# Kernel tuning notes

Measured on AMD Instinct MI355X. Metric: run time of the kernel, lower is better.

The kernel has to match this reference:

```python
import jax, jax.numpy as jnp
import numpy as np

B, C, L = 4, 256, 4096
C8 = C // 8

def setup_inputs() -> dict:
    key = jax.random.key(0)
    ks = jax.random.split(key, 8)
    s = 1.0 / np.sqrt(C)
    x = jax.random.normal(ks[0], (B, C, L), dtype=jnp.float32)
    Wq = jax.random.normal(ks[1], (C8, C), dtype=jnp.float32) * s
    bq = jax.random.normal(ks[2], (C8,), dtype=jnp.float32) * s
    Wk = jax.random.normal(ks[3], (C8, C), dtype=jnp.float32) * s
    bk = jax.random.normal(ks[4], (C8,), dtype=jnp.float32) * s
    Wv = jax.random.normal(ks[5], (C, C), dtype=jnp.float32) * s
    bv = jax.random.normal(ks[6], (C,), dtype=jnp.float32) * s
    gamma = jax.random.normal(ks[7], (1,), dtype=jnp.float32) * 0.1
    return {"x": x, "Wq": Wq, "bq": bq, "Wk": Wk, "bk": bk, "Wv": Wv, "bv": bv, "gamma": gamma}

def reference(x, Wq, bq, Wk, bk, Wv, bv, gamma):
    # pointwise conv1d == channel matmul: [O,C] x [B,C,L] -> [B,O,L]
    q = jnp.einsum('oc,bcl->bol', Wq, x) + bq[None, :, None]   # [B, C8, L]
    k = jnp.einsum('oc,bcl->bol', Wk, x) + bk[None, :, None]   # [B, C8, L]
    v = jnp.einsum('oc,bcl->bol', Wv, x) + bv[None, :, None]   # [B, C,  L]
    # attention[b,i,j] = sum_c q[b,c,i] * k[b,c,j]
    attn = jnp.einsum('bci,bcj->bij', q, k)                    # [B, L, L]
    attn = jax.nn.softmax(attn, axis=-1)
    # out[b,c,i] = sum_j v[b,c,j] * attn[b,i,j]
    out = jnp.einsum('bcj,bij->bci', v, attn)                  # [B, C, L]
    return gamma * out + x
```

## Files before the change

kernel.cpp:

```cpp
#include <hip/hip_runtime.h>
#include <math.h>

#define BB 4
#define CC 256
#define LL 4096
#define DD 32
#define LOG2E 1.44269504088896f

typedef __attribute__((ext_vector_type(8))) short short8;
typedef __attribute__((ext_vector_type(4))) short short4v;
typedef __attribute__((ext_vector_type(4))) float f32x4;
typedef __attribute__((ext_vector_type(4))) unsigned int uint4v;
typedef __attribute__((ext_vector_type(2))) unsigned int uint2v;

#define BARRIER() asm volatile("s_waitcnt lgkmcnt(0)\n\ts_barrier" ::: "memory")

__device__ inline unsigned short f2bf(float f) {
  union { float f; unsigned u; } v; v.f = f;
  unsigned r = v.u + 0x7fffu + ((v.u >> 16) & 1u);
  return (unsigned short)(r >> 16);
}

__device__ inline float fast_exp2(float x) {
#if __has_builtin(__builtin_amdgcn_exp2f)
  return __builtin_amdgcn_exp2f(x);
#else
  return exp2f(x);
#endif
}

__device__ __host__ inline int sigma32(int p) {
  const int q4 = (p >> 3) & 3, u = p & 7;
  return 16 * (u >> 2) + 4 * q4 + (u & 3);
}

__global__ __launch_bounds__(256) void wprep_kernel(
    const float* __restrict__ Wq, const float* __restrict__ Wk, const float* __restrict__ Wv,
    unsigned short* __restrict__ wf)
{
  const int t = threadIdx.x;
  const int ot = blockIdx.x >> 1;
  const int rep = blockIdx.x & 1;
  const int lane = t & 63, cl = lane & 15, q4 = lane >> 4;
  const int ks = (t >> 6) + 4 * rep;
  const int o = ot * 16 + cl;
  const int c = ks * 32 + q4 * 8;
  const float* src = (o < 32) ? (Wq + o * CC) : (o < 64) ? (Wk + (o - 32) * CC)
                                              : (Wv + (o - 64) * CC);
  const float sc = (o < 32) ? LOG2E : 1.0f;
  unsigned short p[8];
  #pragma unroll
  for (int j = 0; j < 8; ++j) p[j] = f2bf(src[c + j] * sc);
  uint4v u;
  u.x = (unsigned)p[0] | ((unsigned)p[1] << 16);
  u.y = (unsigned)p[2] | ((unsigned)p[3] << 16);
  u.z = (unsigned)p[4] | ((unsigned)p[5] << 16);
  u.w = (unsigned)p[6] | ((unsigned)p[7] << 16);
  *(uint4v*)(wf + ((size_t)(ot * 8 + ks) * 64 + lane) * 8) = u;
}

__global__ __launch_bounds__(512, 4) void qkv_kernel(
    const float* __restrict__ x, const unsigned short* __restrict__ wf,
    const float* __restrict__ bq, const float* __restrict__ bk, const float* __restrict__ bv,
    unsigned short* __restrict__ qT, unsigned short* __restrict__ kT,
    unsigned short* __restrict__ vf)
{
  __shared__ union {
    float xl[32 * 261];
    struct {
      unsigned short qk[32 * 72];
      __align__(16) unsigned short v[256 * 40];
    } ep;
  } sm;

  const int t = threadIdx.x;
  const int lane = t & 63, cl = lane & 15, q4 = lane >> 4;
  const int blk = blockIdx.x;
  const int b  = (blk & 7) >> 1;
  const int it = ((blk >> 3) << 1) + (blk & 1);
  const int i0 = it * 32;

  {
    const int ln8 = t & 7;
    #pragma unroll
    for (int p = 0; p < 4; ++p) {
      const int c = (t >> 3) + 64 * p;
      const f32x4 v = *(const f32x4*)(x + ((size_t)(b * CC + c)) * LL + i0 + ln8 * 4);
      #pragma unroll
      for (int k = 0; k < 4; ++k) sm.xl[(ln8 * 4 + k) * 261 + c] = v[k];
    }
  }
  __syncthreads();

  const int wi = (t >> 6) & 1, wo = t >> 7;
  const f32x4 zero = {0.f, 0.f, 0.f, 0.f};
  f32x4 acc[5];
  #pragma unroll
  for (int u = 0; u < 5; ++u) acc[u] = zero;

  for (int ks = 0; ks < 8; ++ks) {
    unsigned short p[8];
    #pragma unroll
    for (int j = 0; j < 8; ++j)
      p[j] = f2bf(sm.xl[(16 * wi + cl) * 261 + ks * 32 + q4 * 8 + j]);
    union { short8 s; uint4v u; } bfr;
    bfr.u.x = (unsigned)p[0] | ((unsigned)p[1] << 16);
    bfr.u.y = (unsigned)p[2] | ((unsigned)p[3] << 16);
    bfr.u.z = (unsigned)p[4] | ((unsigned)p[5] << 16);
    bfr.u.w = (unsigned)p[6] | ((unsigned)p[7] << 16);
    #pragma unroll
    for (int u = 0; u < 5; ++u) {
      const short8 a = *(const short8*)(wf + ((size_t)((wo * 5 + u) * 8 + ks) * 64 + lane) * 8);
      acc[u] = __builtin_amdgcn_mfma_f32_16x16x32_bf16(a, bfr.s, acc[u], 0, 0, 0);
    }
  }
  __syncthreads();

  #pragma unroll
  for (int u = 0; u < 5; ++u) {
    const int g = wo * 5 + u;
    if (g < 4) {
      short4v pk;
      #pragma unroll
      for (int r = 0; r < 4; ++r) {
        const int o = 16 * g + 4 * q4 + r;
        const float v = acc[u][r] + ((o < 32) ? bq[o] * LOG2E : bk[o - 32]);
        pk[r] = (short)f2bf(v);
      }
      *(short4v*)&sm.ep.qk[(16 * wi + cl) * 72 + 16 * g + 4 * q4] = pk;
    } else {
      #pragma unroll
      for (int r = 0; r < 4; ++r) {
        const int ch = 16 * (g - 4) + 4 * q4 + r;
        sm.ep.v[ch * 40 + 16 * wi + cl] = f2bf(acc[u][r] + bv[ch]);
      }
    }
  }
  __syncthreads();

  if (t < 64) {
    const int i = t >> 1, which = t & 1;
    const int gi = i0 + i;
    const unsigned short* srcp = &sm.ep.qk[i * 72 + which * 32];
    uint4v d0 = *(const uint4v*)(srcp + 0);
    uint4v d1 = *(const uint4v*)(srcp + 8);
    uint4v d2 = *(const uint4v*)(srcp + 16);
    uint4v d3 = *(const uint4v*)(srcp + 24);
    unsigned short* dst;
    if (which == 0) {
      dst = qT + ((size_t)b * LL + gi) * DD;
    } else {
      const int row = (gi & ~31) + sigma32(gi & 31);
      dst = kT + ((size_t)b * LL + row) * DD;
    }
    *(uint4v*)dst = d0; *(uint4v*)(dst + 8) = d1;
    *(uint4v*)(dst + 16) = d2; *(uint4v*)(dst + 24) = d3;
  }
  const int kk = it & 1, jt = it >> 1;
  #pragma unroll
  for (int rep = 0; rep < 2; ++rep) {
    const int slot = t + 512 * rep;
    const int fl = slot >> 6, l2 = slot & 63;
    const int cl2 = l2 & 15, q42 = l2 >> 4;
    const int m4 = fl >> 2, mt = fl & 3;
    const int fg = 8 * m4 + 4 * kk + mt;
    const int ch = 64 * m4 + 16 * mt + cl2;
    const uint4v d = *(const uint4v*)&sm.ep.v[ch * 40 + q42 * 8];
    *(uint4v*)(vf + (((size_t)(b * 64 + jt)) * 32 + fg) * 512 + l2 * 8) = d;
  }
}

__global__ __launch_bounds__(512, 2) void attn_kernel(
    const unsigned short* __restrict__ qT, const unsigned short* __restrict__ kT,
    const unsigned short* __restrict__ vf, const float* __restrict__ x,
    const float* __restrict__ gamma_p, float* __restrict__ out)
{
  __shared__ union __align__(16) {
    unsigned short P[2][8][4][2][64][4];
    float Om[4][16][64][4];
  } sm;
  __shared__ float l_lds[8][4][64];

  const int t = threadIdx.x;
  const int w = t >> 6, lane = t & 63, cl = lane & 15, q4 = lane >> 4;
  const int m4 = w & 3, kh = w >> 2;
  const int blk = blockIdx.x;
  const int b  = (blk & 7) >> 1;
  const int it = ((blk >> 3) << 1) + (blk & 1);
  const int i0 = it * 64;

  short8 qa[4];
  #pragma unroll
  for (int nt = 0; nt < 4; ++nt)
    qa[nt] = *(const short8*)(qT + ((size_t)b * LL + i0 + 16 * nt + cl) * DD + q4 * 8);

  const f32x4 zero = {0.f, 0.f, 0.f, 0.f};
  f32x4 O[4][4];
  #pragma unroll
  for (int mt = 0; mt < 4; ++mt)
    #pragma unroll
    for (int nt = 0; nt < 4; ++nt) O[mt][nt] = zero;
  float l_r[4] = {0.f, 0.f, 0.f, 0.f};

  const unsigned short* kbase = kT + ((size_t)b * LL + 32 * w + cl) * DD + q4 * 8;
  const unsigned short* vroot = vf + ((size_t)(b * 64)) * 32 * 512 + lane * 8;

  short8 kb[2];
  #pragma unroll
  for (int h = 0; h < 2; ++h)
    kb[h] = *(const short8*)(kbase + (size_t)(16 * h) * DD);

  short8 va[2][4];
  #pragma unroll
  for (int e = 0; e < 2; ++e) {
    const int kk = 4 * kh + e;
    const size_t base = ((size_t)((kk >> 1) * 32) + 8 * m4 + 4 * (kk & 1)) * 512;
    #pragma unroll
    for (int mt = 0; mt < 4; ++mt)
      va[e][mt] = *(const short8*)(vroot + base + mt * 512);
  }

  for (int ss = 0; ss < 16; ++ss) {
    const int buf = ss & 1;

    f32x4 s[2][4];
    __builtin_amdgcn_s_setprio(1);
    #pragma unroll
    for (int h = 0; h < 2; ++h)
      #pragma unroll
      for (int nt = 0; nt < 4; ++nt)
        s[h][nt] = __builtin_amdgcn_mfma_f32_16x16x32_bf16(kb[h], qa[nt], zero, 0, 0, 0);
    __builtin_amdgcn_s_setprio(0);
    #pragma unroll
    for (int h = 0; h < 2; ++h)
      kb[h] = *(const short8*)(kbase + (size_t)(((ss + 1) & 15) * 256 + 16 * h) * DD);

    #pragma unroll
    for (int h = 0; h < 2; ++h)
      #pragma unroll
      for (int nt = 0; nt < 4; ++nt) {
        const float e0 = fast_exp2(s[h][nt][0]);
        const float e1 = fast_exp2(s[h][nt][1]);
        const float e2 = fast_exp2(s[h][nt][2]);
        const float e3 = fast_exp2(s[h][nt][3]);
        uint2v uv;
        uv.x = __builtin_amdgcn_perm(__float_as_uint(e1), __float_as_uint(e0), 0x07060302);
        uv.y = __builtin_amdgcn_perm(__float_as_uint(e3), __float_as_uint(e2), 0x07060302);
        *(uint2v*)&sm.P[buf][w][nt][h][lane][0] = uv;
        l_r[nt] += (e0 + e1) + (e2 + e3);
      }
    BARRIER();

    #pragma unroll
    for (int e = 0; e < 4; ++e) {
      const int kk = 4 * kh + e;
      short8 pb[4];
      #pragma unroll
      for (int nt = 0; nt < 4; ++nt) {
        union { short8 s8; uint2v h[2]; } pbu;
        pbu.h[0] = *(const uint2v*)&sm.P[buf][kk][nt][0][lane][0];
        pbu.h[1] = *(const uint2v*)&sm.P[buf][kk][nt][1][lane][0];
        pb[nt] = pbu.s8;
      }
      __builtin_amdgcn_s_setprio(1);
      #pragma unroll
      for (int mt = 0; mt < 4; ++mt)
        #pragma unroll
        for (int nt = 0; nt < 4; ++nt)
          O[mt][nt] = __builtin_amdgcn_mfma_f32_16x16x32_bf16(va[e & 1][mt], pb[nt],
                                                              O[mt][nt], 0, 0, 0);
      __builtin_amdgcn_s_setprio(0);
      const int nss = (e < 2) ? ss : ((ss + 1) & 15);
      const int nkk = (e < 2) ? (kk + 2) : (4 * kh + (e - 2));
      const size_t base = ((size_t)(nss * 4 + (nkk >> 1)) * 32 + 8 * m4 + 4 * (nkk & 1)) * 512;
      #pragma unroll
      for (int mt = 0; mt < 4; ++mt)
        va[e & 1][mt] = *(const short8*)(vroot + base + mt * 512);
    }
  }

  #pragma unroll
  for (int nt = 0; nt < 4; ++nt)
    l_lds[w][nt][lane] = l_r[nt];
  BARRIER();
  if (kh == 1) {
    #pragma unroll
    for (int mt = 0; mt < 4; ++mt)
      #pragma unroll
      for (int nt = 0; nt < 4; ++nt)
        *(f32x4*)&sm.Om[m4][mt * 4 + nt][lane][0] = O[mt][nt];
  }
  BARRIER();
  if (kh == 0) {
    const float gam = gamma_p[0];
    float inv_l[4];
    #pragma unroll
    for (int nt = 0; nt < 4; ++nt) {
      float s = 0.f;
      #pragma unroll
      for (int sl = 0; sl < 8; ++sl)
        #pragma unroll
        for (int g = 0; g < 4; ++g)
          s += l_lds[sl][nt][g * 16 + cl];
      inv_l[nt] = 1.0f / s;
    }
    #pragma unroll
    for (int mt = 0; mt < 4; ++mt) {
      #pragma unroll
      for (int nt = 0; nt < 4; ++nt) {
        const f32x4 om = *(const f32x4*)&sm.Om[m4][mt * 4 + nt][lane][0];
        #pragma unroll
        for (int r = 0; r < 4; ++r) {
          const int ch = 64 * m4 + 16 * mt + 4 * q4 + r;
          const int i  = i0 + 16 * nt + cl;
          const size_t idx = ((size_t)b * CC + ch) * LL + i;
          out[idx] = gam * (O[mt][nt][r] + om[r]) * inv_l[nt] + x[idx];
        }
      }
    }
  }
}

extern "C" void kernel_launch(void* const* d_in, const int* in_sizes, int n_in,
                              void* d_out, int out_size, void* d_ws, size_t ws_size,
                              hipStream_t stream) {
  const float* x     = (const float*)d_in[0];
  const float* Wq    = (const float*)d_in[1];
  const float* bq    = (const float*)d_in[2];
  const float* Wk    = (const float*)d_in[3];
  const float* bk    = (const float*)d_in[4];
  const float* Wv    = (const float*)d_in[5];
  const float* bv    = (const float*)d_in[6];
  const float* gamma = (const float*)d_in[7];
  float* out = (float*)d_out;

  unsigned short* qT = (unsigned short*)d_ws;
  unsigned short* kT = qT + (size_t)BB * LL * DD;
  unsigned short* vf = kT + (size_t)BB * LL * DD;
  unsigned short* wf = (unsigned short*)d_out;

  wprep_kernel<<<40, 256, 0, stream>>>(Wq, Wk, Wv, wf);
  qkv_kernel<<<512, 512, 0, stream>>>(x, wf, bq, bk, bv, qT, kT, vf);
  attn_kernel<<<256, 512, 0, stream>>>(qT, kT, vf, x, gamma, out);
}
```

Baseline: 132.4 us.

## Split attention work across 16 waves per block with staged O reduction

```diff
diff --git a/kernel.cpp b/kernel.cpp
--- a/kernel.cpp
+++ b/kernel.cpp
@@ -170,29 +170,33 @@
   }
 }
 
-__global__ __launch_bounds__(512, 2) void attn_kernel(
+__global__ __launch_bounds__(1024, 4) void attn_kernel(
     const unsigned short* __restrict__ qT, const unsigned short* __restrict__ kT,
     const unsigned short* __restrict__ vf, const float* __restrict__ x,
     const float* __restrict__ gamma_p, float* __restrict__ out)
 {
   __shared__ union __align__(16) {
     unsigned short P[2][8][4][2][64][4];
-    float Om[4][16][64][4];
+    float OmA[2][4][16][64][4];
   } sm;
-  __shared__ float l_lds[8][4][64];
+  __shared__ float l_lds[16][4][64];
+  __shared__ float l2[4][4][64];
+  __shared__ __align__(16) unsigned short qls[4 * 64 * 8];
 
   const int t = threadIdx.x;
   const int w = t >> 6, lane = t & 63, cl = lane & 15, q4 = lane >> 4;
-  const int m4 = w & 3, kh = w >> 2;
+  const int kk_a = w & 7, ha = w >> 3;
+  const int m4 = w & 3, kp = w >> 2;
   const int blk = blockIdx.x;
   const int b  = (blk & 7) >> 1;
   const int it = ((blk >> 3) << 1) + (blk & 1);
   const int i0 = it * 64;
 
-  short8 qa[4];
-  #pragma unroll
-  for (int nt = 0; nt < 4; ++nt)
-    qa[nt] = *(const short8*)(qT + ((size_t)b * LL + i0 + 16 * nt + cl) * DD + q4 * 8);
+  if (t < 256) {
+    const int nt = t >> 6, lq = t & 63, clq = lq & 15, q4q = lq >> 4;
+    *(uint4v*)&qls[t * 8] =
+        *(const uint4v*)(qT + ((size_t)b * LL + i0 + 16 * nt + clq) * DD + q4q * 8);
+  }
 
   const f32x4 zero = {0.f, 0.f, 0.f, 0.f};
   f32x4 O[4][4];
@@ -202,58 +206,50 @@
     for (int nt = 0; nt < 4; ++nt) O[mt][nt] = zero;
   float l_r[4] = {0.f, 0.f, 0.f, 0.f};
 
-  const unsigned short* kbase = kT + ((size_t)b * LL + 32 * w + cl) * DD + q4 * 8;
+  const unsigned short* kbase =
+      kT + ((size_t)b * LL + 32 * kk_a + 16 * ha + cl) * DD + q4 * 8;
   const unsigned short* vroot = vf + ((size_t)(b * 64)) * 32 * 512 + lane * 8;
 
-  short8 kb[2];
-  #pragma unroll
-  for (int h = 0; h < 2; ++h)
-    kb[h] = *(const short8*)(kbase + (size_t)(16 * h) * DD);
-
-  short8 va[2][4];
-  #pragma unroll
-  for (int e = 0; e < 2; ++e) {
-    const int kk = 4 * kh + e;
-    const size_t base = ((size_t)((kk >> 1) * 32) + 8 * m4 + 4 * (kk & 1)) * 512;
+  short8 kb = *(const short8*)kbase;
+  short8 va[4];
+  {
+    const int g = 2 * kp;
+    const size_t base = ((size_t)(g >> 1) * 32 + 8 * m4 + 4 * (g & 1)) * 512;
     #pragma unroll
     for (int mt = 0; mt < 4; ++mt)
-      va[e][mt] = *(const short8*)(vroot + base + mt * 512);
-  }
+      va[mt] = *(const short8*)(vroot + base + mt * 512);
+  }
+  __syncthreads();
 
   for (int ss = 0; ss < 16; ++ss) {
     const int buf = ss & 1;
 
-    f32x4 s[2][4];
+    f32x4 s[4];
     __builtin_amdgcn_s_setprio(1);
     #pragma unroll
-    for (int h = 0; h < 2; ++h)
-      #pragma unroll
-      for (int nt = 0; nt < 4; ++nt)
-        s[h][nt] = __builtin_amdgcn_mfma_f32_16x16x32_bf16(kb[h], qa[nt], zero, 0, 0, 0);
+    for (int nt = 0; nt < 4; ++nt)
+      s[nt] = __builtin_amdgcn_mfma_f32_16x16x32_bf16(
+          kb, *(const short8*)&qls[(nt * 64 + lane) * 8], zero, 0, 0, 0);
     __builtin_amdgcn_s_setprio(0);
-    #pragma unroll
-    for (int h = 0; h < 2; ++h)
-      kb[h] = *(const short8*)(kbase + (size_t)(((ss + 1) & 15) * 256 + 16 * h) * DD);
-
-    #pragma unroll
-    for (int h = 0; h < 2; ++h)
-      #pragma unroll
-      for (int nt = 0; nt < 4; ++nt) {
-        const float e0 = fast_exp2(s[h][nt][0]);
-        const float e1 = fast_exp2(s[h][nt][1]);
-        const float e2 = fast_exp2(s[h][nt][2]);
-        const float e3 = fast_exp2(s[h][nt][3]);
-        uint2v uv;
-        uv.x = __builtin_amdgcn_perm(__float_as_uint(e1), __float_as_uint(e0), 0x07060302);
-        uv.y = __builtin_amdgcn_perm(__float_as_uint(e3), __float_as_uint(e2), 0x07060302);
-        *(uint2v*)&sm.P[buf][w][nt][h][lane][0] = uv;
-        l_r[nt] += (e0 + e1) + (e2 + e3);
-      }
+    kb = *(const short8*)(kbase + (size_t)(((ss + 1) & 15) * 256) * DD);
+
+    #pragma unroll
+    for (int nt = 0; nt < 4; ++nt) {
+      const float e0 = fast_exp2(s[nt][0]);
+      const float e1 = fast_exp2(s[nt][1]);
+      const float e2 = fast_exp2(s[nt][2]);
+      const float e3 = fast_exp2(s[nt][3]);
+      uint2v uv;
+      uv.x = __builtin_amdgcn_perm(__float_as_uint(e1), __float_as_uint(e0), 0x07060302);
+      uv.y = __builtin_amdgcn_perm(__float_as_uint(e3), __float_as_uint(e2), 0x07060302);
+      *(uint2v*)&sm.P[buf][kk_a][nt][ha][lane][0] = uv;
+      l_r[nt] += (e0 + e1) + (e2 + e3);
+    }
     BARRIER();
 
     #pragma unroll
-    for (int e = 0; e < 4; ++e) {
-      const int kk = 4 * kh + e;
+    for (int e = 0; e < 2; ++e) {
+      const int kk = 2 * kp + e;
       short8 pb[4];
       #pragma unroll
       for (int nt = 0; nt < 4; ++nt) {
@@ -267,15 +263,15 @@
       for (int mt = 0; mt < 4; ++mt)
         #pragma unroll
         for (int nt = 0; nt < 4; ++nt)
-          O[mt][nt] = __builtin_amdgcn_mfma_f32_16x16x32_bf16(va[e & 1][mt], pb[nt],
+          O[mt][nt] = __builtin_amdgcn_mfma_f32_16x16x32_bf16(va[mt], pb[nt],
                                                               O[mt][nt], 0, 0, 0);
       __builtin_amdgcn_s_setprio(0);
-      const int nss = (e < 2) ? ss : ((ss + 1) & 15);
-      const int nkk = (e < 2) ? (kk + 2) : (4 * kh + (e - 2));
-      const size_t base = ((size_t)(nss * 4 + (nkk >> 1)) * 32 + 8 * m4 + 4 * (nkk & 1)) * 512;
+      const int nss = e ? ((ss + 1) & 15) : ss;
+      const int g = nss * 8 + 2 * kp + (e ^ 1);
+      const size_t base = ((size_t)(g >> 1) * 32 + 8 * m4 + 4 * (g & 1)) * 512;
       #pragma unroll
       for (int mt = 0; mt < 4; ++mt)
-        va[e & 1][mt] = *(const short8*)(vroot + base + mt * 512);
+        va[mt] = *(const short8*)(vroot + base + mt * 512);
     }
   }
 
@@ -283,32 +279,55 @@
   for (int nt = 0; nt < 4; ++nt)
     l_lds[w][nt][lane] = l_r[nt];
   BARRIER();
-  if (kh == 1) {
+
+  {
+    const int ntp = w >> 2, part = w & 3;
+    float sl = l_lds[part * 4 + 0][ntp][lane] + l_lds[part * 4 + 1][ntp][lane]
+             + l_lds[part * 4 + 2][ntp][lane] + l_lds[part * 4 + 3][ntp][lane];
+    l2[part][ntp][lane] = sl;
+  }
+  if (kp >= 2) {
     #pragma unroll
     for (int mt = 0; mt < 4; ++mt)
       #pragma unroll
       for (int nt = 0; nt < 4; ++nt)
-        *(f32x4*)&sm.Om[m4][mt * 4 + nt][lane][0] = O[mt][nt];
+        *(f32x4*)&sm.OmA[kp - 2][m4][mt * 4 + nt][lane][0] = O[mt][nt];
   }
   BARRIER();
-  if (kh == 0) {
+  if (kp < 2) {
+    #pragma unroll
+    for (int mt = 0; mt < 4; ++mt)
+      #pragma unroll
+      for (int nt = 0; nt < 4; ++nt)
+        O[mt][nt] += *(const f32x4*)&sm.OmA[kp][m4][mt * 4 + nt][lane][0];
+  }
+  BARRIER();
+  if (kp == 1) {
+    #pragma unroll
+    for (int mt = 0; mt < 4; ++mt)
+      #pragma unroll
+      for (int nt = 0; nt < 4; ++nt)
+        *(f32x4*)&sm.OmA[0][m4][mt * 4 + nt][lane][0] = O[mt][nt];
+  }
+  BARRIER();
+  if (kp == 0) {
     const float gam = gamma_p[0];
     float inv_l[4];
     #pragma unroll
     for (int nt = 0; nt < 4; ++nt) {
       float s = 0.f;
       #pragma unroll
-      for (int sl = 0; sl < 8; ++sl)
+      for (int part = 0; part < 4; ++part)
         #pragma unroll
         for (int g = 0; g < 4; ++g)
-          s += l_lds[sl][nt][g * 16 + cl];
+          s += l2[part][nt][g * 16 + cl];
       inv_l[nt] = 1.0f / s;
     }
     #pragma unroll
     for (int mt = 0; mt < 4; ++mt) {
       #pragma unroll
       for (int nt = 0; nt < 4; ++nt) {
-        const f32x4 om = *(const f32x4*)&sm.Om[m4][mt * 4 + nt][lane][0];
+        const f32x4 om = *(const f32x4*)&sm.OmA[0][m4][mt * 4 + nt][lane][0];
         #pragma unroll
         for (int r = 0; r < 4; ++r) {
           const int ch = 64 * m4 + 16 * mt + 4 * q4 + r;
@@ -341,5 +360,5 @@
 
   wprep_kernel<<<40, 256, 0, stream>>>(Wq, Wk, Wv, wf);
   qkv_kernel<<<512, 512, 0, stream>>>(x, wf, bq, bk, bv, qT, kT, vf);
-  attn_kernel<<<256, 512, 0, stream>>>(qT, kT, vf, x, gamma, out);
-}
+  attn_kernel<<<256, 1024, 0, stream>>>(qT, kT, vf, x, gamma, out);
+}
```

Measured after the change: 136.1 us. +2.8%, slower.

## Warp-specialize attention kernel into producer and consumer wavefronts

Applied to the files above, without the earlier changes.

```diff
diff --git a/kernel.cpp b/kernel.cpp
--- a/kernel.cpp
+++ b/kernel.cpp
@@ -170,151 +170,149 @@
   }
 }
 
-__global__ __launch_bounds__(512, 2) void attn_kernel(
+__global__ __launch_bounds__(768, 3) void attn_kernel(
     const unsigned short* __restrict__ qT, const unsigned short* __restrict__ kT,
     const unsigned short* __restrict__ vf, const float* __restrict__ x,
     const float* __restrict__ gamma_p, float* __restrict__ out)
 {
-  __shared__ union __align__(16) {
-    unsigned short P[2][8][4][2][64][4];
-    float Om[4][16][64][4];
-  } sm;
+  __shared__ __align__(16) unsigned short P[2][8][4][64][8];
   __shared__ float l_lds[8][4][64];
 
   const int t = threadIdx.x;
   const int w = t >> 6, lane = t & 63, cl = lane & 15, q4 = lane >> 4;
-  const int m4 = w & 3, kh = w >> 2;
   const int blk = blockIdx.x;
   const int b  = (blk & 7) >> 1;
   const int it = ((blk >> 3) << 1) + (blk & 1);
   const int i0 = it * 64;
-
-  short8 qa[4];
-  #pragma unroll
-  for (int nt = 0; nt < 4; ++nt)
-    qa[nt] = *(const short8*)(qT + ((size_t)b * LL + i0 + 16 * nt + cl) * DD + q4 * 8);
-
   const f32x4 zero = {0.f, 0.f, 0.f, 0.f};
-  f32x4 O[4][4];
-  #pragma unroll
-  for (int mt = 0; mt < 4; ++mt)
-    #pragma unroll
-    for (int nt = 0; nt < 4; ++nt) O[mt][nt] = zero;
-  float l_r[4] = {0.f, 0.f, 0.f, 0.f};
-
-  const unsigned short* kbase = kT + ((size_t)b * LL + 32 * w + cl) * DD + q4 * 8;
-  const unsigned short* vroot = vf + ((size_t)(b * 64)) * 32 * 512 + lane * 8;
-
-  short8 kb[2];
-  #pragma unroll
-  for (int h = 0; h < 2; ++h)
-    kb[h] = *(const short8*)(kbase + (size_t)(16 * h) * DD);
-
-  short8 va[2][4];
-  #pragma unroll
-  for (int e = 0; e < 2; ++e) {
-    const int kk = 4 * kh + e;
-    const size_t base = ((size_t)((kk >> 1) * 32) + 8 * m4 + 4 * (kk & 1)) * 512;
-    #pragma unroll
-    for (int mt = 0; mt < 4; ++mt)
-      va[e][mt] = *(const short8*)(vroot + base + mt * 512);
-  }
-
-  for (int ss = 0; ss < 16; ++ss) {
-    const int buf = ss & 1;
-
-    f32x4 s[2][4];
-    __builtin_amdgcn_s_setprio(1);
-    #pragma unroll
-    for (int h = 0; h < 2; ++h)
+
+  if (w < 8) {
+    const int pw = w;
+    short8 qa[4];
+    #pragma unroll
+    for (int nt = 0; nt < 4; ++nt)
+      qa[nt] = *(const short8*)(qT + ((size_t)b * LL + i0 + 16 * nt + cl) * DD + q4 * 8);
+    const unsigned short* kbase =
+        kT + ((size_t)b * LL + 32 * pw + cl) * DD + q4 * 8;
+    short8 kb0 = *(const short8*)kbase;
+    short8 kb1 = *(const short8*)(kbase + (size_t)16 * DD);
+    float l_r[4] = {0.f, 0.f, 0.f, 0.f};
+
+    auto produce = [&](int ss, int buf) {
+      f32x4 s0[4], s1[4];
       #pragma unroll
       for (int nt = 0; nt < 4; ++nt)
-        s[h][nt] = __builtin_amdgcn_mfma_f32_16x16x32_bf16(kb[h], qa[nt], zero, 0, 0, 0);
-    __builtin_amdgcn_s_setprio(0);
-    #pragma unroll
-    for (int h = 0; h < 2; ++h)
-      kb[h] = *(const short8*)(kbase + (size_t)(((ss + 1) & 15) * 256 + 16 * h) * DD);
-
-    #pragma unroll
-    for (int h = 0; h < 2; ++h)
+        s0[nt] = __builtin_amdgcn_mfma_f32_16x16x32_bf16(kb0, qa[nt], zero, 0, 0, 0);
+      #pragma unroll
+      for (int nt = 0; nt < 4; ++nt)
+        s1[nt] = __builtin_amdgcn_mfma_f32_16x16x32_bf16(kb1, qa[nt], zero, 0, 0, 0);
+      const int nss = (ss + 1) & 15;
+      kb0 = *(const short8*)(kbase + (size_t)(nss * 256) * DD);
+      kb1 = *(const short8*)(kbase + (size_t)(nss * 256 + 16) * DD);
       #pragma unroll
       for (int nt = 0; nt < 4; ++nt) {
-        const float e0 = fast_exp2(s[h][nt][0]);
-        const float e1 = fast_exp2(s[h][nt][1]);
-        const float e2 = fast_exp2(s[h][nt][2]);
-        const float e3 = fast_exp2(s[h][nt][3]);
-        uint2v uv;
-        uv.x = __builtin_amdgcn_perm(__float_as_uint(e1), __float_as_uint(e0), 0x07060302);
-        uv.y = __builtin_amdgcn_perm(__float_as_uint(e3), __float_as_uint(e2), 0x07060302);
-        *(uint2v*)&sm.P[buf][w][nt][h][lane][0] = uv;
-        l_r[nt] += (e0 + e1) + (e2 + e3);
-      }
+        const float a0 = fast_exp2(s0[nt][0]);
+        const float a1 = fast_exp2(s0[nt][1]);
+        const float a2 = fast_exp2(s0[nt][2]);
+        const float a3 = fast_exp2(s0[nt][3]);
+        const float b0 = fast_exp2(s1[nt][0]);
+        const float b1 = fast_exp2(s1[nt][1]);
+        const float b2 = fast_exp2(s1[nt][2]);
+        const float b3 = fast_exp2(s1[nt][3]);
+        uint4v u;
+        u.x = __builtin_amdgcn_perm(__float_as_uint(a1), __float_as_uint(a0), 0x07060302);
+        u.y = __builtin_amdgcn_perm(__float_as_uint(a3), __float_as_uint(a2), 0x07060302);
+        u.z = __builtin_amdgcn_perm(__float_as_uint(b1), __float_as_uint(b0), 0x07060302);
+        u.w = __builtin_amdgcn_perm(__float_as_uint(b3), __float_as_uint(b2), 0x07060302);
+        *(uint4v*)&P[buf][pw][nt][lane][0] = u;
+        l_r[nt] += ((a0 + a1) + (a2 + a3)) + ((b0 + b1) + (b2 + b3));
+      }
+    };
+
+    produce(0, 0);
+    __syncthreads();
+    for (int i = 0; i < 16; ++i) {
+      if (i < 15) produce(i + 1, (i + 1) & 1);
+      BARRIER();
+    }
+    #pragma unroll
+    for (int nt = 0; nt < 4; ++nt)
+      l_lds[pw][nt][lane] = l_r[nt];
     BARRIER();
-
-    #pragma unroll
-    for (int e = 0; e < 4; ++e) {
-      const int kk = 4 * kh + e;
-      short8 pb[4];
-      #pragma unroll
-      for (int nt = 0; nt < 4; ++nt) {
-        union { short8 s8; uint2v h[2]; } pbu;
-        pbu.h[0] = *(const uint2v*)&sm.P[buf][kk][nt][0][lane][0];
-        pbu.h[1] = *(const uint2v*)&sm.P[buf][kk][nt][1][lane][0];
-        pb[nt] = pbu.s8;
-      }
-      __builtin_amdgcn_s_setprio(1);
-      #pragma unroll
-      for (int mt = 0; mt < 4; ++mt)
+  } else {
+    const int mq = w - 8;
+    const unsigned short* vroot = vf + ((size_t)(b * 64)) * 32 * 512 + lane * 8;
+    f32x4 O[4][4];
+    #pragma unroll
+    for (int j = 0; j < 4; ++j)
+      #pragma unroll
+      for (int nt = 0; nt < 4; ++nt) O[j][nt] = zero;
+
+    short8 va[2][4];
+    #pragma unroll
+    for (int s = 0; s < 2; ++s) {
+      const int g = s;
+      const size_t base = ((size_t)(g >> 1) * 32 + 8 * mq + 4 * (g & 1)) * 512;
+      #pragma unroll
+      for (int j = 0; j < 4; ++j)
+        va[s][j] = *(const short8*)(vroot + base + j * 512);
+    }
+    __syncthreads();
+
+    for (int i = 0; i < 16; ++i) {
+      const int buf = i & 1;
+      short8 pb[2][4];
+      #pragma unroll
+      for (int nt = 0; nt < 4; ++nt)
+        pb[0][nt] = *(const short8*)&P[buf][0][nt][lane][0];
+      #pragma unroll
+      for (int e = 0; e < 8; ++e) {
+        const int cs = e & 1;
+        if (e < 7) {
+          #pragma unroll
+          for (int nt = 0; nt < 4; ++nt)
+            pb[cs ^ 1][nt] = *(const short8*)&P[buf][e + 1][nt][lane][0];
+        }
+        __builtin_amdgcn_s_setprio(1);
         #pragma unroll
-        for (int nt = 0; nt < 4; ++nt)
-          O[mt][nt] = __builtin_amdgcn_mfma_f32_16x16x32_bf16(va[e & 1][mt], pb[nt],
-                                                              O[mt][nt], 0, 0, 0);
-      __builtin_amdgcn_s_setprio(0);
-      const int nss = (e < 2) ? ss : ((ss + 1) & 15);
-      const int nkk = (e < 2) ? (kk + 2) : (4 * kh + (e - 2));
-      const size_t base = ((size_t)(nss * 4 + (nkk >> 1)) * 32 + 8 * m4 + 4 * (nkk & 1)) * 512;
-      #pragma unroll
-      for (int mt = 0; mt < 4; ++mt)
-        va[e & 1][mt] = *(const short8*)(vroot + base + mt * 512);
-    }
-  }
-
-  #pragma unroll
-  for (int nt = 0; nt < 4; ++nt)
-    l_lds[w][nt][lane] = l_r[nt];
-  BARRIER();
-  if (kh == 1) {
-    #pragma unroll
-    for (int mt = 0; mt < 4; ++mt)
-      #pragma unroll
-      for (int nt = 0; nt < 4; ++nt)
-        *(f32x4*)&sm.Om[m4][mt * 4 + nt][lane][0] = O[mt][nt];
-  }
-  BARRIER();
-  if (kh == 0) {
+        for (int j = 0; j < 4; ++j)
+          #pragma unroll
+          for (int nt = 0; nt < 4; ++nt)
+            O[j][nt] = __builtin_amdgcn_mfma_f32_16x16x32_bf16(va[e & 1][j], pb[cs][nt],
+                                                               O[j][nt], 0, 0, 0);
+        __builtin_amdgcn_s_setprio(0);
+        const int g2 = (8 * i + e + 2) & 127;
+        const size_t base = ((size_t)(g2 >> 1) * 32 + 8 * mq + 4 * (g2 & 1)) * 512;
+        #pragma unroll
+        for (int j = 0; j < 4; ++j)
+          va[e & 1][j] = *(const short8*)(vroot + base + j * 512);
+      }
+      BARRIER();
+    }
+    BARRIER();
+
     const float gam = gamma_p[0];
     float inv_l[4];
     #pragma unroll
     for (int nt = 0; nt < 4; ++nt) {
       float s = 0.f;
       #pragma unroll
-      for (int sl = 0; sl < 8; ++sl)
+      for (int pw = 0; pw < 8; ++pw)
         #pragma unroll
         for (int g = 0; g < 4; ++g)
-          s += l_lds[sl][nt][g * 16 + cl];
+          s += l_lds[pw][nt][g * 16 + cl];
       inv_l[nt] = 1.0f / s;
     }
     #pragma unroll
-    for (int mt = 0; mt < 4; ++mt) {
+    for (int j = 0; j < 4; ++j) {
       #pragma unroll
       for (int nt = 0; nt < 4; ++nt) {
-        const f32x4 om = *(const f32x4*)&sm.Om[m4][mt * 4 + nt][lane][0];
         #pragma unroll
         for (int r = 0; r < 4; ++r) {
-          const int ch = 64 * m4 + 16 * mt + 4 * q4 + r;
+          const int ch = 64 * mq + 16 * j + 4 * q4 + r;
           const int i  = i0 + 16 * nt + cl;
           const size_t idx = ((size_t)b * CC + ch) * LL + i;
-          out[idx] = gam * (O[mt][nt][r] + om[r]) * inv_l[nt] + x[idx];
+          out[idx] = gam * O[j][nt][r] * inv_l[nt] + x[idx];
         }
       }
     }
@@ -341,5 +339,5 @@
 
   wprep_kernel<<<40, 256, 0, stream>>>(Wq, Wk, Wv, wf);
   qkv_kernel<<<512, 512, 0, stream>>>(x, wf, bq, bk, bv, qT, kT, vf);
-  attn_kernel<<<256, 512, 0, stream>>>(qT, kT, vf, x, gamma, out);
-}
+  attn_kernel<<<256, 768, 0, stream>>>(qT, kT, vf, x, gamma, out);
+}
```

Result: no change. 131.6 us (-0.5%).
